# Kernel optimization log

Measured on AMD Instinct MI355X. Metric: run time of the kernel, lower is better.

The kernel has to match this reference:

```python
import jax, jax.numpy as jnp
import numpy as np

# Graph sizes: 3-hop neighbor-sampled minibatch (PyG NeighborSampler layout)
N0, N1, N2, N3 = 1_000_000, 100_000, 10_000, 1024   # node counts per hop
E0, E1, E2 = 1_500_000, 150_000, 15_360             # edge counts per hop
D, H = 128, 512                                     # in_out_channels, hidden_channels


def setup_inputs() -> dict:
    key = jax.random.key(0)
    ks = jax.random.split(key, 16)

    def lin(k, fi, fo):  # Glorot-ish init for a Linear weight (in, out)
        return jax.random.normal(k, (fi, fo), jnp.float32) / np.sqrt(fi).astype(np.float32)

    return {
        "x": jax.random.normal(ks[0], (N0, D), jnp.float32),
        "ei0_src": jax.random.randint(ks[1], (E0,), 0, N0),
        "ei0_dst": jax.random.randint(ks[2], (E0,), 0, N1),
        "ei1_src": jax.random.randint(ks[3], (E1,), 0, N1),
        "ei1_dst": jax.random.randint(ks[4], (E1,), 0, N2),
        "ei2_src": jax.random.randint(ks[5], (E2,), 0, N2),
        "ei2_dst": jax.random.randint(ks[6], (E2,), 0, N3),
        "W_l0": lin(ks[7], D, H), "b_l0": jnp.zeros((H,), jnp.float32), "W_r0": lin(ks[8], D, H),
        "W_l1": lin(ks[9], H, H), "b_l1": jnp.zeros((H,), jnp.float32), "W_r1": lin(ks[10], H, H),
        "W_l2": lin(ks[11], H, D), "b_l2": jnp.zeros((D,), jnp.float32), "W_r2": lin(ks[12], H, D),
    }


def _sage_conv(x_src, n_tgt, src, dst, W_l, b_l, W_r):
    """PyG SAGEConv (mean aggr): lin_l(scatter_mean(x_src[src] -> dst)) + lin_r(x_tgt)."""
    x_tgt = x_src[:n_tgt]                       # targets are the first n_tgt nodes
    msg = x_src[src]                            # [E, F_in] neighbor gather
    agg_sum = jax.ops.segment_sum(msg, dst, num_segments=n_tgt)
    cnt = jax.ops.segment_sum(jnp.ones((src.shape[0], 1), msg.dtype), dst, num_segments=n_tgt)
    agg_mean = agg_sum / jnp.maximum(cnt, 1.0)
    return agg_mean @ W_l + b_l + x_tgt @ W_r


def reference(x, ei0_src, ei0_dst, ei1_src, ei1_dst, ei2_src, ei2_dst,
              W_l0, b_l0, W_r0, W_l1, b_l1, W_r1, W_l2, b_l2, W_r2):
    h = _sage_conv(x, N1, ei0_src, ei0_dst, W_l0, b_l0, W_r0)
    h = jax.nn.gelu(h, approximate=False)       # F.gelu (exact erf); eval-mode dropout = identity
    h = _sage_conv(h, N2, ei1_src, ei1_dst, W_l1, b_l1, W_r1)
    h = jax.nn.gelu(h, approximate=False)
    h = _sage_conv(h, N3, ei2_src, ei2_dst, W_l2, b_l2, W_r2)
    return h  # [N3, D]
```

## Files before the change

### kernel.cpp

```cpp
#include <hip/hip_runtime.h>
#include <math.h>

static const int N0 = 1000000, N1 = 100000, N2 = 10000, N3 = 1024;
static const int E0 = 1500000, E1 = 150000, E2 = 15360;
static const int D = 128, H = 512;

typedef unsigned short u16;
typedef __attribute__((ext_vector_type(8))) short bf16x8;
typedef __attribute__((ext_vector_type(4))) float f32x4;
typedef __attribute__((ext_vector_type(4))) unsigned short us4;
typedef __attribute__((ext_vector_type(4))) int i32x4;

__global__ void count_kernel(const int* __restrict__ dst, int* __restrict__ cnt, int E) {
    int e = blockIdx.x * blockDim.x + threadIdx.x;
    if (e < E) atomicAdd(cnt + dst[e], 1);
}

__global__ __launch_bounds__(1024)
void scan_kernel(const int* __restrict__ cnt, int* __restrict__ offs, int N, int E) {
    __shared__ int part[1024];
    int t = threadIdx.x;
    int per = (N + 1023) >> 10;
    int beg = t * per, end = min(beg + per, N);
    int s = 0;
    for (int i = beg; i < end; ++i) s += cnt[i];
    part[t] = s;
    __syncthreads();
    for (int off = 1; off < 1024; off <<= 1) {
        int v = (t >= off) ? part[t - off] : 0;
        __syncthreads();
        part[t] += v;
        __syncthreads();
    }
    int run = (t == 0) ? 0 : part[t - 1];
    for (int i = beg; i < end; ++i) { offs[i] = run; run += cnt[i]; }
    if (t == 0) offs[N] = E;
}

__global__ void fill_kernel(const int* __restrict__ dst, const int* __restrict__ src,
                            const int* __restrict__ offs, int* __restrict__ cur,
                            int* __restrict__ sorted, int E) {
    int e = blockIdx.x * blockDim.x + threadIdx.x;
    if (e < E) {
        int d = dst[e];
        int p = offs[d] + atomicAdd(cur + d, 1);
        sorted[p] = src[e];
    }
}

__global__ __launch_bounds__(256)
void gather_mean_128(const float* __restrict__ x, const int* __restrict__ offs,
                     const int* __restrict__ srt, float* __restrict__ agg, int Ntgt) {
    int wid = (int)((blockIdx.x * 256 + threadIdx.x) >> 6);
    int lane = threadIdx.x & 63;
    if (wid >= Ntgt) return;
    int beg = offs[wid], end = offs[wid + 1];
    float ax = 0.f, ay = 0.f;
    int e = beg;
    for (; e + 4 <= end; e += 4) {
        int s0 = srt[e], s1 = srt[e + 1], s2 = srt[e + 2], s3 = srt[e + 3];
        float2 v0 = ((const float2*)(x + (size_t)s0 * 128))[lane];
        float2 v1 = ((const float2*)(x + (size_t)s1 * 128))[lane];
        float2 v2 = ((const float2*)(x + (size_t)s2 * 128))[lane];
        float2 v3 = ((const float2*)(x + (size_t)s3 * 128))[lane];
        ax += v0.x + v1.x + v2.x + v3.x;
        ay += v0.y + v1.y + v2.y + v3.y;
    }
    for (; e < end; ++e) {
        int s = srt[e];
        float2 v = ((const float2*)(x + (size_t)s * 128))[lane];
        ax += v.x; ay += v.y;
    }
    float inv = 1.0f / (float)max(end - beg, 1);
    ((float2*)(agg + (size_t)wid * 128))[lane] = make_float2(ax * inv, ay * inv);
}

__global__ __launch_bounds__(256)
void gather_mean_512(const float* __restrict__ x, const int* __restrict__ offs,
                     const int* __restrict__ srt, float* __restrict__ agg, int Ntgt) {
    int gw = (int)((blockIdx.x * 256 + threadIdx.x) >> 6);
    int lane = threadIdx.x & 63;
    int node = gw >> 1, half = gw & 1;
    if (node >= Ntgt) return;
    int beg = offs[node], end = offs[node + 1];
    int co = half * 256 + lane * 4;
    float4 acc = make_float4(0.f, 0.f, 0.f, 0.f);
    int e = beg;
    for (; e + 4 <= end; e += 4) {
        int s0 = srt[e], s1 = srt[e + 1], s2 = srt[e + 2], s3 = srt[e + 3];
        float4 v0 = *(const float4*)(x + (size_t)s0 * 512 + co);
        float4 v1 = *(const float4*)(x + (size_t)s1 * 512 + co);
        float4 v2 = *(const float4*)(x + (size_t)s2 * 512 + co);
        float4 v3 = *(const float4*)(x + (size_t)s3 * 512 + co);
        acc.x += v0.x + v1.x + v2.x + v3.x;
        acc.y += v0.y + v1.y + v2.y + v3.y;
        acc.z += v0.z + v1.z + v2.z + v3.z;
        acc.w += v0.w + v1.w + v2.w + v3.w;
    }
    for (; e < end; ++e) {
        int s = srt[e];
        float4 v = *(const float4*)(x + (size_t)s * 512 + co);
        acc.x += v.x; acc.y += v.y; acc.z += v.z; acc.w += v.w;
    }
    float inv = 1.0f / (float)max(end - beg, 1);
    acc.x *= inv; acc.y *= inv; acc.z *= inv; acc.w *= inv;
    *(float4*)(agg + (size_t)node * 512 + co) = acc;
}

__device__ __forceinline__ u16 bhi(float v) {
    return (u16)(__float_as_uint(v) >> 16);
}
__device__ __forceinline__ u16 blo(float v) {
    float hf = __uint_as_float(__float_as_uint(v) & 0xFFFF0000u);
    return (u16)(__float_as_uint(v - hf) >> 16);
}

__global__ void wsplit_kernel(const float* __restrict__ W, u16* __restrict__ bt,
                              int K, int N) {
    int idx = blockIdx.x * 256 + threadIdx.x;
    if (idx >= K * N) return;
    int k = idx / N, n = idx - k * N;
    float v = W[idx];
    bt[(size_t)n * K + k] = bhi(v);
    bt[(size_t)N * K + (size_t)n * K + k] = blo(v);
}

#define LDK 40

template <bool GELU>
__global__ __launch_bounds__(256)
void combine_mfma(const float* __restrict__ A0, const float* __restrict__ A1,
                  const u16* __restrict__ Bt0, const u16* __restrict__ Bt1,
                  const float* __restrict__ bias, float* __restrict__ out,
                  int M, int K, int N) {
    __shared__ u16 As_hi[128][LDK];
    __shared__ u16 As_lo[128][LDK];
    __shared__ u16 Bs_hi[128][LDK];
    __shared__ u16 Bs_lo[128][LDK];

    int t = threadIdx.x;
    int lane = t & 63, wid = t >> 6;
    int wm = (wid >> 1) * 64, wn = (wid & 1) * 64;
    int m0 = blockIdx.y * 128, n0 = blockIdx.x * 128;

    int ar = t >> 3;
    int akq = (t & 7) * 4;
    int bn = t >> 2;
    int bc = (t & 3) * 8;

    int fr = lane & 15, kg = lane >> 4;

    f32x4 acc[4][4] = {};

    for (int p = 0; p < 2; ++p) {
        const float* A  = p ? A1 : A0;
        const u16*   Bh = p ? Bt1 : Bt0;
        const u16*   Bl = Bh + (size_t)N * K;

        for (int k0 = 0; k0 < K; k0 += 32) {
#pragma unroll
            for (int it = 0; it < 4; ++it) {
                int row = it * 32 + ar;
                int rg = m0 + row;
                f32x4 v = {0.f, 0.f, 0.f, 0.f};
                if (rg < M) v = *(const f32x4*)(A + (size_t)rg * K + k0 + akq);
                us4 hv = { bhi(v.x), bhi(v.y), bhi(v.z), bhi(v.w) };
                us4 lv = { blo(v.x), blo(v.y), blo(v.z), blo(v.w) };
                *(us4*)&As_hi[row][akq] = hv;
                *(us4*)&As_lo[row][akq] = lv;
            }
#pragma unroll
            for (int it = 0; it < 2; ++it) {
                int nn = it * 64 + bn;
                size_t goff = (size_t)(n0 + nn) * K + k0 + bc;
                *(i32x4*)&Bs_hi[nn][bc] = *(const i32x4*)(Bh + goff);
                *(i32x4*)&Bs_lo[nn][bc] = *(const i32x4*)(Bl + goff);
            }
            __syncthreads();

            bf16x8 a_hi[4], a_lo[4], b_hi[4], b_lo[4];
#pragma unroll
            for (int i = 0; i < 4; ++i) {
                a_hi[i] = *(const bf16x8*)&As_hi[wm + i * 16 + fr][kg * 8];
                a_lo[i] = *(const bf16x8*)&As_lo[wm + i * 16 + fr][kg * 8];
                b_hi[i] = *(const bf16x8*)&Bs_hi[wn + i * 16 + fr][kg * 8];
                b_lo[i] = *(const bf16x8*)&Bs_lo[wn + i * 16 + fr][kg * 8];
            }
#pragma unroll
            for (int i = 0; i < 4; ++i)
#pragma unroll
                for (int j = 0; j < 4; ++j) {
                    acc[i][j] = __builtin_amdgcn_mfma_f32_16x16x32_bf16(
                        a_hi[i], b_hi[j], acc[i][j], 0, 0, 0);
                    acc[i][j] = __builtin_amdgcn_mfma_f32_16x16x32_bf16(
                        a_hi[i], b_lo[j], acc[i][j], 0, 0, 0);
                    acc[i][j] = __builtin_amdgcn_mfma_f32_16x16x32_bf16(
                        a_lo[i], b_hi[j], acc[i][j], 0, 0, 0);
                }
            __syncthreads();
        }
    }

    int fq = lane >> 4;
#pragma unroll
    for (int i = 0; i < 4; ++i) {
        int rbase = m0 + wm + i * 16 + fq * 4;
#pragma unroll
        for (int j = 0; j < 4; ++j) {
            int c = n0 + wn + j * 16 + fr;
            float bv = bias[c];
#pragma unroll
            for (int r = 0; r < 4; ++r) {
                int row = rbase + r;
                if (row < M) {
                    float v = acc[i][j][r] + bv;
                    if (GELU) v = 0.5f * v * (1.0f + erff(v * 0.70710678118654752f));
                    out[(size_t)row * N + c] = v;
                }
            }
        }
    }
}

extern "C" void kernel_launch(void* const* d_in, const int* in_sizes, int n_in,
                              void* d_out, int out_size, void* d_ws, size_t ws_size,
                              hipStream_t stream) {
    const float* x       = (const float*)d_in[0];
    const int*   ei0_src = (const int*)d_in[1];
    const int*   ei0_dst = (const int*)d_in[2];
    const int*   ei1_src = (const int*)d_in[3];
    const int*   ei1_dst = (const int*)d_in[4];
    const int*   ei2_src = (const int*)d_in[5];
    const int*   ei2_dst = (const int*)d_in[6];
    const float* W_l0    = (const float*)d_in[7];
    const float* b_l0    = (const float*)d_in[8];
    const float* W_r0    = (const float*)d_in[9];
    const float* W_l1    = (const float*)d_in[10];
    const float* b_l1    = (const float*)d_in[11];
    const float* W_r1    = (const float*)d_in[12];
    const float* W_l2    = (const float*)d_in[13];
    const float* b_l2    = (const float*)d_in[14];
    const float* W_r2    = (const float*)d_in[15];
    float* out = (float*)d_out;
    float* ws  = (float*)d_ws;

    float* h1 = ws;
    int* offs0 = (int*)ws;
    int* cnt0  = offs0 + (N1 + 1);
    int* cur0  = cnt0 + N1;
    int* srt0  = cur0 + N1;

    float* agg0 = h1 + (size_t)N1 * H;
    float* agg1 = agg0;
    float* h2   = agg1 + (size_t)N2 * H;
    float* agg2 = h2 + (size_t)N2 * H;

    u16* bt1l = (u16*)(agg2 + (size_t)N3 * H);
    u16* bt1r = bt1l + (size_t)H * H * 2;
    u16* bt2l = bt1r + (size_t)H * H * 2;
    u16* bt2r = bt2l + (size_t)D * H * 2;

    u16* bt0l = (u16*)d_out;
    u16* bt0r = bt0l + (size_t)H * D * 2;

    int* tail  = (int*)(agg0 + (size_t)N1 * D);
    int* offs1 = tail;
    int* cnt1  = offs1 + (N2 + 1);
    int* cur1  = cnt1 + N2;
    int* srt1  = cur1 + N2;
    int* offs2 = srt1 + E1;
    int* cnt2  = offs2 + (N3 + 1);
    int* cur2  = cnt2 + N3;
    int* srt2  = cur2 + N3;

    hipMemsetAsync(cnt0, 0, 2 * N1 * sizeof(int), stream);
    hipMemsetAsync(cnt1, 0, 2 * N2 * sizeof(int), stream);
    hipMemsetAsync(cnt2, 0, 2 * N3 * sizeof(int), stream);
    count_kernel<<<(E0 + 255) / 256, 256, 0, stream>>>(ei0_dst, cnt0, E0);
    count_kernel<<<(E1 + 255) / 256, 256, 0, stream>>>(ei1_dst, cnt1, E1);
    count_kernel<<<(E2 + 255) / 256, 256, 0, stream>>>(ei2_dst, cnt2, E2);
    scan_kernel<<<1, 1024, 0, stream>>>(cnt0, offs0, N1, E0);
    scan_kernel<<<1, 1024, 0, stream>>>(cnt1, offs1, N2, E1);
    scan_kernel<<<1, 1024, 0, stream>>>(cnt2, offs2, N3, E2);
    fill_kernel<<<(E0 + 255) / 256, 256, 0, stream>>>(ei0_dst, ei0_src, offs0, cur0, srt0, E0);
    fill_kernel<<<(E1 + 255) / 256, 256, 0, stream>>>(ei1_dst, ei1_src, offs1, cur1, srt1, E1);
    fill_kernel<<<(E2 + 255) / 256, 256, 0, stream>>>(ei2_dst, ei2_src, offs2, cur2, srt2, E2);

    wsplit_kernel<<<(D * H + 255) / 256, 256, 0, stream>>>(W_l0, bt0l, D, H);
    wsplit_kernel<<<(D * H + 255) / 256, 256, 0, stream>>>(W_r0, bt0r, D, H);

    gather_mean_128<<<(N1 + 3) / 4, 256, 0, stream>>>(x, offs0, srt0, agg0, N1);
    combine_mfma<true><<<dim3(H / 128, (N1 + 127) / 128), 256, 0, stream>>>(
        agg0, x, bt0l, bt0r, b_l0, h1, N1, D, H);

    wsplit_kernel<<<(H * H + 255) / 256, 256, 0, stream>>>(W_l1, bt1l, H, H);
    wsplit_kernel<<<(H * H + 255) / 256, 256, 0, stream>>>(W_r1, bt1r, H, H);
    wsplit_kernel<<<(H * D + 255) / 256, 256, 0, stream>>>(W_l2, bt2l, H, D);
    wsplit_kernel<<<(H * D + 255) / 256, 256, 0, stream>>>(W_r2, bt2r, H, D);

    gather_mean_512<<<(2 * N2 + 3) / 4, 256, 0, stream>>>(h1, offs1, srt1, agg1, N2);
    combine_mfma<true><<<dim3(H / 128, (N2 + 127) / 128), 256, 0, stream>>>(
        agg1, h1, bt1l, bt1r, b_l1, h2, N2, H, H);

    gather_mean_512<<<(2 * N3 + 3) / 4, 256, 0, stream>>>(h2, offs2, srt2, agg2, N3);
    combine_mfma<false><<<dim3(D / 128, (N3 + 127) / 128), 256, 0, stream>>>(
        agg2, h2, bt2l, bt2r, b_l2, out, N3, H, D);
}
```

Measured before the change: 1.525 ms.

## Pre-split activations into bf16 hi/lo planes and add smaller GEMM tile variant

The gather kernels now write their mean aggregates directly as separate bf16 hi/lo planes, and separate split kernels convert the target-node rows (x, h1, h2) into the same format. The GEMM then loads pre-split bf16 data instead of converting fp32 in its inner loop. A BM=64 tile variant is added for the smaller layers to get more blocks, and the gather unroll goes from 4 to 8. This adds extra passes over x and h to split them, and the workspace is reorganised with an aligned bump allocator.

```diff
diff --git a/kernel.cpp b/kernel.cpp
--- a/kernel.cpp
+++ b/kernel.cpp
@@ -6,10 +6,19 @@
 static const int D = 128, H = 512;
 
 typedef unsigned short u16;
+typedef unsigned int u32;
 typedef __attribute__((ext_vector_type(8))) short bf16x8;
 typedef __attribute__((ext_vector_type(4))) float f32x4;
 typedef __attribute__((ext_vector_type(4))) unsigned short us4;
 typedef __attribute__((ext_vector_type(4))) int i32x4;
+
+__device__ __forceinline__ u16 bhi(float v) {
+    return (u16)(__float_as_uint(v) >> 16);
+}
+__device__ __forceinline__ u16 blo(float v) {
+    float hf = __uint_as_float(__float_as_uint(v) & 0xFFFF0000u);
+    return (u16)(__float_as_uint(v - hf) >> 16);
+}
 
 __global__ void count_kernel(const int* __restrict__ dst, int* __restrict__ cnt, int E) {
     int e = blockIdx.x * blockDim.x + threadIdx.x;
@@ -48,23 +57,49 @@
     }
 }
 
+__global__ void split_rows_kernel(const float* __restrict__ src, u16* __restrict__ dst,
+                                  int total) {
+    int i = (blockIdx.x * 256 + threadIdx.x) * 4;
+    if (i >= total) return;
+    f32x4 v = *(const f32x4*)(src + i);
+    us4 hv = { bhi(v.x), bhi(v.y), bhi(v.z), bhi(v.w) };
+    us4 lv = { blo(v.x), blo(v.y), blo(v.z), blo(v.w) };
+    *(us4*)(dst + i) = hv;
+    *(us4*)(dst + (size_t)total + i) = lv;
+}
+
+__global__ void wsplit_kernel(const float* __restrict__ W, u16* __restrict__ bt,
+                              int K, int N) {
+    int idx = blockIdx.x * 256 + threadIdx.x;
+    if (idx >= K * N) return;
+    int k = idx / N, n = idx - k * N;
+    float v = W[idx];
+    bt[(size_t)n * K + k] = bhi(v);
+    bt[(size_t)N * K + (size_t)n * K + k] = blo(v);
+}
+
 __global__ __launch_bounds__(256)
-void gather_mean_128(const float* __restrict__ x, const int* __restrict__ offs,
-                     const int* __restrict__ srt, float* __restrict__ agg, int Ntgt) {
+void gather_mean_128p(const float* __restrict__ x, const int* __restrict__ offs,
+                      const int* __restrict__ srt, u16* __restrict__ aggP, int Ntgt) {
     int wid = (int)((blockIdx.x * 256 + threadIdx.x) >> 6);
     int lane = threadIdx.x & 63;
     if (wid >= Ntgt) return;
     int beg = offs[wid], end = offs[wid + 1];
     float ax = 0.f, ay = 0.f;
     int e = beg;
-    for (; e + 4 <= end; e += 4) {
+    for (; e + 8 <= end; e += 8) {
         int s0 = srt[e], s1 = srt[e + 1], s2 = srt[e + 2], s3 = srt[e + 3];
+        int s4 = srt[e + 4], s5 = srt[e + 5], s6 = srt[e + 6], s7 = srt[e + 7];
         float2 v0 = ((const float2*)(x + (size_t)s0 * 128))[lane];
         float2 v1 = ((const float2*)(x + (size_t)s1 * 128))[lane];
         float2 v2 = ((const float2*)(x + (size_t)s2 * 128))[lane];
         float2 v3 = ((const float2*)(x + (size_t)s3 * 128))[lane];
-        ax += v0.x + v1.x + v2.x + v3.x;
-        ay += v0.y + v1.y + v2.y + v3.y;
+        float2 v4 = ((const float2*)(x + (size_t)s4 * 128))[lane];
+        float2 v5 = ((const float2*)(x + (size_t)s5 * 128))[lane];
+        float2 v6 = ((const float2*)(x + (size_t)s6 * 128))[lane];
+        float2 v7 = ((const float2*)(x + (size_t)s7 * 128))[lane];
+        ax += v0.x + v1.x + v2.x + v3.x + v4.x + v5.x + v6.x + v7.x;
+        ay += v0.y + v1.y + v2.y + v3.y + v4.y + v5.y + v6.y + v7.y;
     }
     for (; e < end; ++e) {
         int s = srt[e];
@@ -72,12 +107,17 @@
         ax += v.x; ay += v.y;
     }
     float inv = 1.0f / (float)max(end - beg, 1);
-    ((float2*)(agg + (size_t)wid * 128))[lane] = make_float2(ax * inv, ay * inv);
+    ax *= inv; ay *= inv;
+    size_t stride = (size_t)Ntgt * 128;
+    u32 hw = (u32)bhi(ax) | ((u32)bhi(ay) << 16);
+    u32 lw = (u32)blo(ax) | ((u32)blo(ay) << 16);
+    ((u32*)aggP)[(size_t)wid * 64 + lane] = hw;
+    ((u32*)(aggP + stride))[(size_t)wid * 64 + lane] = lw;
 }
 
 __global__ __launch_bounds__(256)
-void gather_mean_512(const float* __restrict__ x, const int* __restrict__ offs,
-                     const int* __restrict__ srt, float* __restrict__ agg, int Ntgt) {
+void gather_mean_512p(const float* __restrict__ x, const int* __restrict__ offs,
+                      const int* __restrict__ srt, u16* __restrict__ aggP, int Ntgt) {
     int gw = (int)((blockIdx.x * 256 + threadIdx.x) >> 6);
     int lane = threadIdx.x & 63;
     int node = gw >> 1, half = gw & 1;
@@ -104,92 +144,87 @@
     }
     float inv = 1.0f / (float)max(end - beg, 1);
     acc.x *= inv; acc.y *= inv; acc.z *= inv; acc.w *= inv;
-    *(float4*)(agg + (size_t)node * 512 + co) = acc;
-}
-
-__device__ __forceinline__ u16 bhi(float v) {
-    return (u16)(__float_as_uint(v) >> 16);
-}
-__device__ __forceinline__ u16 blo(float v) {
-    float hf = __uint_as_float(__float_as_uint(v) & 0xFFFF0000u);
-    return (u16)(__float_as_uint(v - hf) >> 16);
-}
-
-__global__ void wsplit_kernel(const float* __restrict__ W, u16* __restrict__ bt,
-                              int K, int N) {
-    int idx = blockIdx.x * 256 + threadIdx.x;
-    if (idx >= K * N) return;
-    int k = idx / N, n = idx - k * N;
-    float v = W[idx];
-    bt[(size_t)n * K + k] = bhi(v);
-    bt[(size_t)N * K + (size_t)n * K + k] = blo(v);
+    size_t stride = (size_t)Ntgt * 512;
+    us4 hv = { bhi(acc.x), bhi(acc.y), bhi(acc.z), bhi(acc.w) };
+    us4 lv = { blo(acc.x), blo(acc.y), blo(acc.z), blo(acc.w) };
+    *(us4*)(aggP + (size_t)node * 512 + co) = hv;
+    *(us4*)(aggP + stride + (size_t)node * 512 + co) = lv;
 }
 
 #define LDK 40
 
-template <bool GELU>
+template <int BM, bool GELU>
 __global__ __launch_bounds__(256)
-void combine_mfma(const float* __restrict__ A0, const float* __restrict__ A1,
+void combine_mfma(const u16* __restrict__ A0P, const u16* __restrict__ A1P,
                   const u16* __restrict__ Bt0, const u16* __restrict__ Bt1,
                   const float* __restrict__ bias, float* __restrict__ out,
                   int M, int K, int N) {
-    __shared__ u16 As_hi[128][LDK];
-    __shared__ u16 As_lo[128][LDK];
+    constexpr int NJ = (BM == 128) ? 4 : 2;
+    __shared__ u16 As_hi[BM][LDK];
+    __shared__ u16 As_lo[BM][LDK];
     __shared__ u16 Bs_hi[128][LDK];
     __shared__ u16 Bs_lo[128][LDK];
 
     int t = threadIdx.x;
     int lane = t & 63, wid = t >> 6;
-    int wm = (wid >> 1) * 64, wn = (wid & 1) * 64;
-    int m0 = blockIdx.y * 128, n0 = blockIdx.x * 128;
-
-    int ar = t >> 3;
-    int akq = (t & 7) * 4;
-    int bn = t >> 2;
-    int bc = (t & 3) * 8;
+    int wm = (BM == 128) ? (wid >> 1) * 64 : 0;
+    int wn = (BM == 128) ? (wid & 1) * 64 : wid * 32;
+    int m0 = blockIdx.y * BM, n0 = blockIdx.x * 128;
+
+    int sr = t >> 2;
+    int sc = (t & 3) * 8;
 
     int fr = lane & 15, kg = lane >> 4;
 
-    f32x4 acc[4][4] = {};
+    f32x4 acc[4][NJ] = {};
+
+    size_t strideA = (size_t)M * K;
+    size_t strideB = (size_t)N * K;
 
     for (int p = 0; p < 2; ++p) {
-        const float* A  = p ? A1 : A0;
-        const u16*   Bh = p ? Bt1 : Bt0;
-        const u16*   Bl = Bh + (size_t)N * K;
+        const u16* Ah = p ? A1P : A0P;
+        const u16* Al = Ah + strideA;
+        const u16* Bh = p ? Bt1 : Bt0;
+        const u16* Bl = Bh + strideB;
 
         for (int k0 = 0; k0 < K; k0 += 32) {
 #pragma unroll
-            for (int it = 0; it < 4; ++it) {
-                int row = it * 32 + ar;
+            for (int it = 0; it < BM / 64; ++it) {
+                int row = it * 64 + sr;
                 int rg = m0 + row;
-                f32x4 v = {0.f, 0.f, 0.f, 0.f};
-                if (rg < M) v = *(const f32x4*)(A + (size_t)rg * K + k0 + akq);
-                us4 hv = { bhi(v.x), bhi(v.y), bhi(v.z), bhi(v.w) };
-                us4 lv = { blo(v.x), blo(v.y), blo(v.z), blo(v.w) };
-                *(us4*)&As_hi[row][akq] = hv;
-                *(us4*)&As_lo[row][akq] = lv;
+                i32x4 hv = {0, 0, 0, 0}, lv = {0, 0, 0, 0};
+                if (rg < M) {
+                    size_t goff = (size_t)rg * K + k0 + sc;
+                    hv = *(const i32x4*)(Ah + goff);
+                    lv = *(const i32x4*)(Al + goff);
+                }
+                *(i32x4*)&As_hi[row][sc] = hv;
+                *(i32x4*)&As_lo[row][sc] = lv;
             }
 #pragma unroll
             for (int it = 0; it < 2; ++it) {
-                int nn = it * 64 + bn;
-                size_t goff = (size_t)(n0 + nn) * K + k0 + bc;
-                *(i32x4*)&Bs_hi[nn][bc] = *(const i32x4*)(Bh + goff);
-                *(i32x4*)&Bs_lo[nn][bc] = *(const i32x4*)(Bl + goff);
+                int nn = it * 64 + sr;
+                size_t goff = (size_t)(n0 + nn) * K + k0 + sc;
+                *(i32x4*)&Bs_hi[nn][sc] = *(const i32x4*)(Bh + goff);
+                *(i32x4*)&Bs_lo[nn][sc] = *(const i32x4*)(Bl + goff);
             }
             __syncthreads();
 
-            bf16x8 a_hi[4], a_lo[4], b_hi[4], b_lo[4];
+            bf16x8 a_hi[4], a_lo[4], b_hi[NJ], b_lo[NJ];
 #pragma unroll
             for (int i = 0; i < 4; ++i) {
                 a_hi[i] = *(const bf16x8*)&As_hi[wm + i * 16 + fr][kg * 8];
                 a_lo[i] = *(const bf16x8*)&As_lo[wm + i * 16 + fr][kg * 8];
-                b_hi[i] = *(const bf16x8*)&Bs_hi[wn + i * 16 + fr][kg * 8];
-                b_lo[i] = *(const bf16x8*)&Bs_lo[wn + i * 16 + fr][kg * 8];
+            }
+#pragma unroll
+            for (int j = 0; j < NJ; ++j) {
+                b_hi[j] = *(const bf16x8*)&Bs_hi[wn + j * 16 + fr][kg * 8];
+                b_lo[j] = *(const bf16x8*)&Bs_lo[wn + j * 16 + fr][kg * 8];
             }
 #pragma unroll
             for (int i = 0; i < 4; ++i)
 #pragma unroll
-                for (int j = 0; j < 4; ++j) {
+                for (int j = 0; j < NJ; ++j) {
                     acc[i][j] = __builtin_amdgcn_mfma_f32_16x16x32_bf16(
                         a_hi[i], b_hi[j], acc[i][j], 0, 0, 0);
                     acc[i][j] = __builtin_amdgcn_mfma_f32_16x16x32_bf16(
@@ -206,7 +241,7 @@
     for (int i = 0; i < 4; ++i) {
         int rbase = m0 + wm + i * 16 + fq * 4;
 #pragma unroll
-        for (int j = 0; j < 4; ++j) {
+        for (int j = 0; j < NJ; ++j) {
             int c = n0 + wn + j * 16 + fr;
             float bv = bias[c];
 #pragma unroll
@@ -242,36 +277,37 @@
     const float* b_l2    = (const float*)d_in[14];
     const float* W_r2    = (const float*)d_in[15];
     float* out = (float*)d_out;
-    float* ws  = (float*)d_ws;
-
-    float* h1 = ws;
-    int* offs0 = (int*)ws;
-    int* cnt0  = offs0 + (N1 + 1);
-    int* cur0  = cnt0 + N1;
-    int* srt0  = cur0 + N1;
-
-    float* agg0 = h1 + (size_t)N1 * H;
-    float* agg1 = agg0;
-    float* h2   = agg1 + (size_t)N2 * H;
-    float* agg2 = h2 + (size_t)N2 * H;
-
-    u16* bt1l = (u16*)(agg2 + (size_t)N3 * H);
-    u16* bt1r = bt1l + (size_t)H * H * 2;
-    u16* bt2l = bt1r + (size_t)H * H * 2;
-    u16* bt2r = bt2l + (size_t)D * H * 2;
-
-    u16* bt0l = (u16*)d_out;
-    u16* bt0r = bt0l + (size_t)H * D * 2;
-
-    int* tail  = (int*)(agg0 + (size_t)N1 * D);
-    int* offs1 = tail;
-    int* cnt1  = offs1 + (N2 + 1);
-    int* cur1  = cnt1 + N2;
-    int* srt1  = cur1 + N2;
-    int* offs2 = srt1 + E1;
-    int* cnt2  = offs2 + (N3 + 1);
-    int* cur2  = cnt2 + N3;
-    int* srt2  = cur2 + N3;
+    char*  ws  = (char*)d_ws;
+
+    size_t off = 0;
+    auto alloc = [&](size_t bytes) { char* p = ws + off; off += (bytes + 255) & ~(size_t)255; return p; };
+
+    float* h1    = (float*)alloc((size_t)N1 * H * 4);
+    float* h2    = (float*)alloc((size_t)N2 * H * 4);
+    u16*   aggP0 = (u16*)alloc((size_t)N1 * D * 2 * 2);
+    u16*   xP0   = (u16*)alloc((size_t)N1 * D * 2 * 2);
+    u16*   aggP1 = (u16*)alloc((size_t)N2 * H * 2 * 2);
+    u16*   h1P   = (u16*)alloc((size_t)N2 * H * 2 * 2);
+    u16*   aggP2 = (u16*)alloc((size_t)N3 * H * 2 * 2);
+    u16*   h2P   = (u16*)alloc((size_t)N3 * H * 2 * 2);
+    u16*   bt0l  = (u16*)alloc((size_t)H * D * 2 * 2);
+    u16*   bt0r  = (u16*)alloc((size_t)H * D * 2 * 2);
+    u16*   bt1l  = (u16*)alloc((size_t)H * H * 2 * 2);
+    u16*   bt1r  = (u16*)alloc((size_t)H * H * 2 * 2);
+    u16*   bt2l  = (u16*)alloc((size_t)D * H * 2 * 2);
+    u16*   bt2r  = (u16*)alloc((size_t)D * H * 2 * 2);
+    int*   offs0 = (int*)alloc((size_t)(N1 + 1) * 4);
+    int*   cnt0  = (int*)alloc((size_t)2 * N1 * 4);
+    int*   srt0  = (int*)alloc((size_t)E0 * 4);
+    int*   offs1 = (int*)alloc((size_t)(N2 + 1) * 4);
+    int*   cnt1  = (int*)alloc((size_t)2 * N2 * 4);
+    int*   srt1  = (int*)alloc((size_t)E1 * 4);
+    int*   offs2 = (int*)alloc((size_t)(N3 + 1) * 4);
+    int*   cnt2  = (int*)alloc((size_t)2 * N3 * 4);
+    int*   srt2  = (int*)alloc((size_t)E2 * 4);
+    int* cur0 = cnt0 + N1;
+    int* cur1 = cnt1 + N2;
+    int* cur2 = cnt2 + N3;
 
     hipMemsetAsync(cnt0, 0, 2 * N1 * sizeof(int), stream);
     hipMemsetAsync(cnt1, 0, 2 * N2 * sizeof(int), stream);
@@ -288,21 +324,23 @@
 
     wsplit_kernel<<<(D * H + 255) / 256, 256, 0, stream>>>(W_l0, bt0l, D, H);
     wsplit_kernel<<<(D * H + 255) / 256, 256, 0, stream>>>(W_r0, bt0r, D, H);
-
-    gather_mean_128<<<(N1 + 3) / 4, 256, 0, stream>>>(x, offs0, srt0, agg0, N1);
-    combine_mfma<true><<<dim3(H / 128, (N1 + 127) / 128), 256, 0, stream>>>(
-        agg0, x, bt0l, bt0r, b_l0, h1, N1, D, H);
-
     wsplit_kernel<<<(H * H + 255) / 256, 256, 0, stream>>>(W_l1, bt1l, H, H);
     wsplit_kernel<<<(H * H + 255) / 256, 256, 0, stream>>>(W_r1, bt1r, H, H);
     wsplit_kernel<<<(H * D + 255) / 256, 256, 0, stream>>>(W_l2, bt2l, H, D);
     wsplit_kernel<<<(H * D + 255) / 256, 256, 0, stream>>>(W_r2, bt2r, H, D);
-
-    gather_mean_512<<<(2 * N2 + 3) / 4, 256, 0, stream>>>(h1, offs1, srt1, agg1, N2);
-    combine_mfma<true><<<dim3(H / 128, (N2 + 127) / 128), 256, 0, stream>>>(
-        agg1, h1, bt1l, bt1r, b_l1, h2, N2, H, H);
-
-    gather_mean_512<<<(2 * N3 + 3) / 4, 256, 0, stream>>>(h2, offs2, srt2, agg2, N3);
-    combine_mfma<false><<<dim3(D / 128, (N3 + 127) / 128), 256, 0, stream>>>(
-        agg2, h2, bt2l, bt2r, b_l2, out, N3, H, D);
-}
+    split_rows_kernel<<<(N1 * D / 4 + 255) / 256, 256, 0, stream>>>(x, xP0, N1 * D);
+
+    gather_mean_128p<<<(N1 + 3) / 4, 256, 0, stream>>>(x, offs0, srt0, aggP0, N1);
+    combine_mfma<128, true><<<dim3(H / 128, (N1 + 127) / 128), 256, 0, stream>>>(
+        aggP0, xP0, bt0l, bt0r, b_l0, h1, N1, D, H);
+
+    split_rows_kernel<<<(N2 * H / 4 + 255) / 256, 256, 0, stream>>>(h1, h1P, N2 * H);
+    gather_mean_512p<<<(2 * N2 + 3) / 4, 256, 0, stream>>>(h1, offs1, srt1, aggP1, N2);
+    combine_mfma<64, true><<<dim3(H / 128, (N2 + 63) / 64), 256, 0, stream>>>(
+        aggP1, h1P, bt1l, bt1r, b_l1, h2, N2, H, H);
+
+    split_rows_kernel<<<(N3 * H / 4 + 255) / 256, 256, 0, stream>>>(h2, h2P, N3 * H);
+    gather_mean_512p<<<(2 * N3 + 3) / 4, 256, 0, stream>>>(h2, offs2, srt2, aggP2, N3);
+    combine_mfma<64, false><<<dim3(D / 128, (N3 + 63) / 64), 256, 0, stream>>>(
+        aggP2, h2P, bt2l, bt2r, b_l2, out, N3, H, D);
+}
```

Result: faster. 1.433 ms (-6.0%).
